# Performance work log

Hardware: AMD Instinct MI355X
Metric: run time of the kernel (lower is better)

Reference implementation:

```python
import jax, jax.numpy as jnp
import numpy as np

H = 128  # hidden_size (hardcoded as hidden_dim=128 in the torch gather)


def _conv1x1(W, b, x):
    # Conv1d kernel_size=1: W [out, in], x [B, in, S] -> [B, out, S]
    return jnp.einsum('oh,bhs->bos', W, x) + b[None, :, None]


def setup_inputs() -> dict:
    key = jax.random.key(0)
    ks = jax.random.split(key, 16)
    B, S = 2048, 128
    sc = 0.05
    inp = {
        'static': jax.random.normal(ks[0], (B, 2, S), jnp.float32),
        'dynamic': jax.random.uniform(ks[1], (B, 2, S), jnp.float32),
        'mark': jnp.zeros((1,), jnp.float32),
        # encoders (Conv1d k=1)
        'W_s': jax.random.normal(ks[2], (H, 2)) * sc, 'b_s': jnp.zeros((H,)),
        'W_ld': jax.random.normal(ks[3], (H, 2)) * sc, 'b_ld': jnp.zeros((H,)),
        'W_d': jax.random.normal(ks[4], (H, 2)) * sc, 'b_d': jnp.zeros((H,)),
        # LSTMCell
        'W_ih': jax.random.normal(ks[5], (4 * H, H)) * sc, 'b_ih': jnp.zeros((4 * H,)),
        'W_hh': jax.random.normal(ks[6], (4 * H, H)) * sc, 'b_hh': jnp.zeros((4 * H,)),
        # pointer projections
        'W_pd': jax.random.normal(ks[7], (H, H)) * sc, 'b_pd': jnp.zeros((H,)),
        'W_pld': jax.random.normal(ks[8], (H, H)) * sc, 'b_pld': jnp.zeros((H,)),
        'W_pq': jax.random.normal(ks[9], (H, H)) * sc, 'b_pq': jnp.zeros((H,)),
        'W_pr': jax.random.normal(ks[10], (H, H)) * sc, 'b_pr': jnp.zeros((H,)),
        # attention vector W (V is unused in the original forward)
        'attn_W': jax.random.normal(ks[11], (1, H)) * sc,
    }
    return inp


def reference(static, dynamic, mark, W_s, b_s, W_ld, b_ld, W_d, b_d,
              W_ih, b_ih, W_hh, b_hh, W_pd, b_pd, W_pld, b_pld,
              W_pq, b_pq, W_pr, b_pr, attn_W):
    B, _, S = static.shape
    static_hidden = _conv1x1(W_s, b_s, static)                 # [B,H,S]
    load, demand = dynamic[:, 0:1, :], dynamic[:, 1:2, :]
    dyn_ld = _conv1x1(W_ld, b_ld, load - demand)               # [B,H,S]
    dyn_d = _conv1x1(W_d, b_d, demand)                         # [B,H,S]
    # loop-invariant projections (recomputed each step in torch; identical math)
    base = (_conv1x1(W_pr, b_pr, static_hidden)
            + _conv1x1(W_pld, b_pld, dyn_ld)
            + _conv1x1(W_pd, b_pd, dyn_d))                     # [B,H,S]

    # mask = [0, 1, 1, ..., 1]; mask_fn is None so it never changes
    mask2 = jnp.concatenate([jnp.zeros((1,), static.dtype),
                             jnp.ones((S - 1,), static.dtype)])

    dec0 = static_hidden[:, :, 0]
    h0 = jnp.zeros((B, H), static.dtype)
    c0 = jnp.zeros((B, H), static.dtype)

    def lstm_cell(x, h, c):
        gates = x @ W_ih.T + b_ih + h @ W_hh.T + b_hh
        i, f, g, o = jnp.split(gates, 4, axis=1)
        c2 = jax.nn.sigmoid(f) * c + jax.nn.sigmoid(i) * jnp.tanh(g)
        h2 = jax.nn.sigmoid(o) * jnp.tanh(c2)
        return h2, c2

    def step(carry, _):
        dec, h, c = carry
        h, c = lstm_cell(dec, h, c)
        q = h @ W_pq.T + b_pq                                  # project_query
        hidden = base + q[:, :, None]                          # [B,H,S]
        attns = jnp.einsum('h,bhs->bs', attn_W[0], jnp.tanh(hidden))
        probs = jax.nn.softmax(attns + 10000.0 * mask2[None, :], axis=1)
        prob = jnp.max(probs, axis=1)                          # greedy (eval path)
        ptr = jnp.argmax(probs, axis=1)
        logp = jnp.log(prob)
        dec2 = jax.lax.stop_gradient(
            jnp.take_along_axis(static_hidden, ptr[:, None, None], axis=2)[:, :, 0])
        return (dec2, h, c), (ptr, logp)

    _, (ptrs, logps) = jax.lax.scan(step, (dec0, h0, c0), None, length=S)
    tour_idx = ptrs.T                                          # [B,S] int
    tour_logp = logps.T                                        # [B,S]
    return tour_idx, tour_logp, mark
```

## Files before the change

kernel.cpp:

```cpp
#include <hip/hip_runtime.h>


#define H 128
#define S 128
#define NBATCH 2048
#define NB 8
#define NT 1024
#define NBLK (NBATCH / NB)
#define BS (NBATCH * S)

#define SHQ 36
#define SHB (4 * SHQ)
#define SHI(bb, h) ((bb) * SHB + (((h) >> 5) * SHQ) + ((h) & 31))
#define QPB 132
#define PADF 12288

typedef float v2f __attribute__((ext_vector_type(2)));
typedef float v4f __attribute__((ext_vector_type(4)));

__device__ __forceinline__ v2f fma2(v2f a, v2f b, v2f c) {
  return __builtin_elementwise_fma(a, b, c);
}
__device__ __forceinline__ v2f splat2(float x) { return (v2f){x, x}; }

__device__ __forceinline__ float dot4f(float4 a, float4 b, float c) {
  return fmaf(a.x, b.x, fmaf(a.y, b.y, fmaf(a.z, b.z, fmaf(a.w, b.w, c))));
}
__device__ __forceinline__ float fast_tanh(float x) {
  float e = __expf(2.f * x);
  float r = __builtin_amdgcn_rcpf(e + 1.f);
  return fmaf(-2.f, r, 1.f);
}
__device__ __forceinline__ float fast_sig(float x) {
  return __builtin_amdgcn_rcpf(1.f + __expf(-x));
}
__device__ __forceinline__ float qsum8(float a) {
  int t;
  t = __builtin_amdgcn_update_dpp(0, __float_as_int(a), 0xB1, 0xF, 0xF, true);
  a += __int_as_float(t);
  t = __builtin_amdgcn_update_dpp(0, __float_as_int(a), 0x4E, 0xF, 0xF, true);
  a += __int_as_float(t);
  a += __shfl_xor(a, 4);
  return a;
}

__global__ __launch_bounds__(NT) __attribute__((amdgpu_waves_per_eu(4, 4)))
void drl4tsp_fused(const float* __restrict__ st, const float* __restrict__ dyn,
                   const float* __restrict__ W_s, const float* __restrict__ b_s,
                   const float* __restrict__ W_ld, const float* __restrict__ b_ld,
                   const float* __restrict__ W_d, const float* __restrict__ b_d,
                   const float* __restrict__ W_ih, const float* __restrict__ b_ih,
                   const float* __restrict__ W_hh, const float* __restrict__ b_hh,
                   const float* __restrict__ W_pd, const float* __restrict__ b_pd,
                   const float* __restrict__ W_pld, const float* __restrict__ b_pld,
                   const float* __restrict__ W_pq, const float* __restrict__ b_pq,
                   const float* __restrict__ W_pr, const float* __restrict__ b_pr,
                   const float* __restrict__ attn_W, const float* __restrict__ mark,
                   float* __restrict__ out)
{
  __shared__ float4 sX[NB][S];
  __shared__ float4 sA[H];
  __shared__ alignas(16) float sAW[H];
  __shared__ float  sQB[H];
  __shared__ float4 sGT4[4][H];
  __shared__ float  sH[NB * SHB];
  __shared__ alignas(16) float sQP[NB * QPB];
  __shared__ float2 sPart[16][64];
  __shared__ float  sOutI[NB][S];
  __shared__ float  sOutL[NB][S];
  __shared__ float  sSelX0[NB];
  __shared__ float  sSelX1[NB];
  __shared__ float  sPad[PADF];

  const int tid = threadIdx.x;
  const int b0  = blockIdx.x * NB;
  const int gg  = tid >> 3, qq = tid & 7;
  const int wv  = tid >> 6, lane = tid & 63;
  const int cb  = wv & 7;
  const int ch  = wv >> 3;

  if (mark[0] > 1e30f) {
    volatile float* vp = sPad;
    vp[tid] = mark[0];
  }

  if (qq == 0) {
    #pragma unroll
    for (int g = 0; g < 4; ++g) {
      const int row = gg + g * H;
      const float* wr = W_ih + row * H;
      float g0 = 0.f, g1 = 0.f, gb = 0.f;
      for (int h = 0; h < H; h += 4) {
        float4 w   = *(const float4*)(wr + h);
        float4 s01 = *(const float4*)(W_s + 2 * h);
        float4 s23 = *(const float4*)(W_s + 2 * h + 4);
        float4 bs  = *(const float4*)(b_s + h);
        g0 = fmaf(w.x, s01.x, fmaf(w.y, s01.z, fmaf(w.z, s23.x, fmaf(w.w, s23.z, g0))));
        g1 = fmaf(w.x, s01.y, fmaf(w.y, s01.w, fmaf(w.z, s23.y, fmaf(w.w, s23.w, g1))));
        gb = fmaf(w.x, bs.x,  fmaf(w.y, bs.y,  fmaf(w.z, bs.z,  fmaf(w.w, bs.w,  gb))));
      }
      sGT4[g][gg] = make_float4(g0, g1, gb + b_ih[row] + b_hh[row], 0.f);
    }
  }
  if (tid < H) {
    const int h = tid;
    float a0 = 0.f, a1 = 0.f, a2 = 0.f, a3 = 0.f, bt = 0.f;
    for (int j = 0; j < H; ++j) {
      float pr  = W_pr[h * H + j];
      float pld = W_pld[h * H + j];
      float pd  = W_pd[h * H + j];
      float2 wsv = *(const float2*)(W_s + 2 * j);
      float2 wld = *(const float2*)(W_ld + 2 * j);
      float2 wd  = *(const float2*)(W_d + 2 * j);
      a0 = fmaf(pr, wsv.x, a0);
      a1 = fmaf(pr, wsv.y, a1);
      a2 = fmaf(pld, wld.x + wld.y, a2);
      a3 = fmaf(pd,  wd.x + wd.y,  a3);
      bt += pr * b_s[j] + pld * b_ld[j] + pd * b_d[j];
    }
    sA[h]  = make_float4(a0, a1, a2, a3);
    sAW[h] = attn_W[h];
    sQB[h] = bt + b_pr[h] + b_pld[h] + b_pd[h] + b_pq[h];
  }
  {
    int i = tid;
    int bb = i >> 7, s = i & (S - 1);
    int go = (b0 + bb) * 2 * S;
    float x0 = st[go + s];
    float x1 = st[go + S + s];
    float ld = dyn[go + s];
    float dm = dyn[go + S + s];
    sX[bb][s] = make_float4(x0, x1, ld - dm, dm);
  }
  for (int i = tid; i < NB * SHB; i += NT) sH[i] = 0.f;
  if (tid < NB) {
    int go = (b0 + tid) * 2 * S;
    sSelX0[tid] = st[go + 0];
    sSelX1[tid] = st[go + S + 0];
  }
  if (blockIdx.x == 0 && tid == 0) out[2 * BS] = mark[0];

  v2f rW01[4][4], rW23[4][4];
  #pragma unroll
  for (int k = 0; k < 4; ++k) {
    const int co = 16 * qq + 4 * k;
    float4 w0 = *(const float4*)(W_hh + (gg        ) * H + co);
    float4 w1 = *(const float4*)(W_hh + (gg +     H) * H + co);
    float4 w2 = *(const float4*)(W_hh + (gg + 2 * H) * H + co);
    float4 w3 = *(const float4*)(W_hh + (gg + 3 * H) * H + co);
    rW01[k][0] = (v2f){w0.x, w1.x}; rW01[k][1] = (v2f){w0.y, w1.y};
    rW01[k][2] = (v2f){w0.z, w1.z}; rW01[k][3] = (v2f){w0.w, w1.w};
    rW23[k][0] = (v2f){w2.x, w3.x}; rW23[k][1] = (v2f){w2.y, w3.y};
    rW23[k][2] = (v2f){w2.z, w3.z}; rW23[k][3] = (v2f){w2.w, w3.w};
  }
  float4 rQ[4];
  {
    const float* wr = W_pq + gg * H + 16 * qq;
    #pragma unroll
    for (int k = 0; k < 4; ++k) rQ[k] = *(const float4*)(wr + 4 * k);
  }
  __syncthreads();

  const int ofsH = ((qq * 16) >> 5) * SHQ + ((qq * 16) & 31);
  const float qb = sQB[gg];
  v2f xx2, xy2, xz2, xw2;
  {
    float4 xA = sX[cb][lane];
    float4 xB = sX[cb][lane + 64];
    xx2 = (v2f){xA.x, xB.x}; xy2 = (v2f){xA.y, xB.y};
    xz2 = (v2f){xA.z, xB.z}; xw2 = (v2f){xA.w, xB.w};
  }
  float cS = 0.f;
  float g4[4] = {0.f, 0.f, 0.f, 0.f};

  #pragma unroll 1
  for (int t = 0; t < S; ++t) {
    {
      const float x0p = sSelX0[qq], x1p = sSelX1[qq];
      float4 t0 = sGT4[0][gg];
      float4 t1 = sGT4[1][gg];
      float4 t2 = sGT4[2][gg];
      float4 t3 = sGT4[3][gg];
      float gi = g4[0] + fmaf(t0.x, x0p, fmaf(t0.y, x1p, t0.z));
      float gf = g4[1] + fmaf(t1.x, x0p, fmaf(t1.y, x1p, t1.z));
      float gc = g4[2] + fmaf(t2.x, x0p, fmaf(t2.y, x1p, t2.z));
      float go = g4[3] + fmaf(t3.x, x0p, fmaf(t3.y, x1p, t3.z));
      cS = fast_sig(gf) * cS + fast_sig(gi) * fast_tanh(gc);
      sH[SHI(qq, gg)] = fast_sig(go) * fast_tanh(cS);
    }
    __syncthreads();

    {
      float qval = 0.f;
      #pragma unroll
      for (int bb = 0; bb < NB; ++bb) {
        float qa = 0.f;
        const float* hp = &sH[bb * SHB + ofsH];
        #pragma unroll
        for (int k = 0; k < 4; ++k)
          qa = dot4f(rQ[k], *(const float4*)(hp + 4 * k), qa);
        qa = qsum8(qa);
        if (qq == bb) qval = qa + qb;
      }
      sQP[qq * QPB + gg] = qval;
    }
    __syncthreads();

    v2f at2 = {0.f, 0.f};
    #pragma unroll 1
    for (int jj = 0; jj < 8; ++jj) {
      v2f a01 = {0.f, 0.f}, a23 = {0.f, 0.f};
      {
        const float* hp = &sH[jj * SHB + ofsH];
        #pragma unroll
        for (int k = 0; k < 4; ++k) {
          v4f hv = *(const v4f*)(hp + 4 * k);
          v2f hx = splat2(hv.x), hy = splat2(hv.y);
          v2f hz = splat2(hv.z), hw = splat2(hv.w);
          a01 = fma2(rW01[k][3], hw, a01);
          a01 = fma2(rW01[k][2], hz, a01);
          a01 = fma2(rW01[k][1], hy, a01);
          a01 = fma2(rW01[k][0], hx, a01);
          a23 = fma2(rW23[k][3], hw, a23);
          a23 = fma2(rW23[k][2], hz, a23);
          a23 = fma2(rW23[k][1], hy, a23);
          a23 = fma2(rW23[k][0], hx, a23);
        }
      }
      {
        const int hbase = 64 * ch + 8 * jj;
        #pragma unroll
        for (int hh = 0; hh < 8; ++hh) {
          const int h = hbase + hh;
          float4 a  = sA[h];
          float  aw = sAW[h];
          float  q  = sQP[cb * QPB + h];
          v2f acc = splat2(q);
          acc = fma2(splat2(a.w), xw2, acc);
          acc = fma2(splat2(a.z), xz2, acc);
          acc = fma2(splat2(a.y), xy2, acc);
          acc = fma2(splat2(a.x), xx2, acc);
          v2f tt = acc + acc;
          v2f e  = (v2f){__expf(tt.x), __expf(tt.y)};
          v2f r  = (v2f){__builtin_amdgcn_rcpf(e.x + 1.f),
                         __builtin_amdgcn_rcpf(e.y + 1.f)};
          v2f th = fma2(splat2(-2.f), r, splat2(1.f));
          at2 = fma2(splat2(aw), th, at2);
        }
      }
      {
        float r0 = qsum8(a01.x);
        float r1 = qsum8(a01.y);
        float r2 = qsum8(a23.x);
        float r3 = qsum8(a23.y);
        if (qq == jj) { g4[0] = r0; g4[1] = r1; g4[2] = r2; g4[3] = r3; }
      }
    }
    sPart[wv][lane] = make_float2(at2.x, at2.y);
    __syncthreads();

    if (wv < 8) {
      float at0 = at2.x, at1 = at2.y;
      float2 o = sPart[wv ^ 8][lane];
      at0 += o.x; at1 += o.y;
      float a0v = at0 + ((lane == 0) ? 0.f : 10000.f);
      float a1v = at1 + 10000.f;
      float v; int idx;
      if (a1v > a0v) { v = a1v; idx = lane + 64; } else { v = a0v; idx = lane; }
      #pragma unroll
      for (int m = 1; m < 64; m <<= 1) {
        float ov = __shfl_xor(v, m);
        int   oi = __shfl_xor(idx, m);
        if (ov > v || (ov == v && oi < idx)) { v = ov; idx = oi; }
      }
      float es = __expf(a0v - v) + __expf(a1v - v);
      #pragma unroll
      for (int m = 1; m < 64; m <<= 1) es += __shfl_xor(es, m);
      if (lane == 0) {
        sOutI[cb][t] = (float)idx;
        sOutL[cb][t] = -__logf(es);
        float4 xv = sX[cb][idx];
        sSelX0[cb] = xv.x;
        sSelX1[cb] = xv.y;
      }
    }
    __syncthreads();
  }

  {
    int bb = tid >> 7, s = tid & (S - 1);
    const int bg = b0 + bb;
    out[bg * S + s]      = sOutI[bb][s];
    out[BS + bg * S + s] = sOutL[bb][s];
  }
}

extern "C" void kernel_launch(void* const* d_in, const int* in_sizes, int n_in,
                              void* d_out, int out_size, void* d_ws, size_t ws_size,
                              hipStream_t stream) {
  const float* st     = (const float*)d_in[0];
  const float* dyn    = (const float*)d_in[1];
  const float* mark   = (const float*)d_in[2];
  const float* W_s    = (const float*)d_in[3];
  const float* b_s    = (const float*)d_in[4];
  const float* W_ld   = (const float*)d_in[5];
  const float* b_ld   = (const float*)d_in[6];
  const float* W_d    = (const float*)d_in[7];
  const float* b_d    = (const float*)d_in[8];
  const float* W_ih   = (const float*)d_in[9];
  const float* b_ih   = (const float*)d_in[10];
  const float* W_hh   = (const float*)d_in[11];
  const float* b_hh   = (const float*)d_in[12];
  const float* W_pd   = (const float*)d_in[13];
  const float* b_pd   = (const float*)d_in[14];
  const float* W_pld  = (const float*)d_in[15];
  const float* b_pld  = (const float*)d_in[16];
  const float* W_pq   = (const float*)d_in[17];
  const float* b_pq   = (const float*)d_in[18];
  const float* W_pr   = (const float*)d_in[19];
  const float* b_pr   = (const float*)d_in[20];
  const float* attn_W = (const float*)d_in[21];
  float* out = (float*)d_out;

  hipLaunchKernelGGL(drl4tsp_fused, dim3(NBLK), dim3(NT), 0, stream,
                     st, dyn, W_s, b_s, W_ld, b_ld, W_d, b_d, W_ih, b_ih,
                     W_hh, b_hh, W_pd, b_pd, W_pld, b_pld, W_pq, b_pq,
                     W_pr, b_pr, attn_W, mark, out);
}
```

Measured before the change: 2.670 ms.

## Move W_hh recurrent matvec after attention, overlapping with argmax reduction phase

The h·W_hh gate matvec is pulled out of the interleaved attention loop and placed after the softmax/argmax section, where it runs in all waves while wave<8 threads finish the reduction. W_hh is now kept as per-gate float4 rows using dot4f instead of packed v2f pairs. The aim is to shorten the attention loop and fill the idle phase before the barrier. In exchange, the attention loop loses the interleaved FMA work that could hide transcendental latency, and register use may change.

```diff
diff --git a/kernel.cpp b/kernel.cpp
--- a/kernel.cpp
+++ b/kernel.cpp
@@ -140,18 +140,12 @@
   }
   if (blockIdx.x == 0 && tid == 0) out[2 * BS] = mark[0];
 
-  v2f rW01[4][4], rW23[4][4];
+  float4 rW[4][4];
   #pragma unroll
-  for (int k = 0; k < 4; ++k) {
-    const int co = 16 * qq + 4 * k;
-    float4 w0 = *(const float4*)(W_hh + (gg        ) * H + co);
-    float4 w1 = *(const float4*)(W_hh + (gg +     H) * H + co);
-    float4 w2 = *(const float4*)(W_hh + (gg + 2 * H) * H + co);
-    float4 w3 = *(const float4*)(W_hh + (gg + 3 * H) * H + co);
-    rW01[k][0] = (v2f){w0.x, w1.x}; rW01[k][1] = (v2f){w0.y, w1.y};
-    rW01[k][2] = (v2f){w0.z, w1.z}; rW01[k][3] = (v2f){w0.w, w1.w};
-    rW23[k][0] = (v2f){w2.x, w3.x}; rW23[k][1] = (v2f){w2.y, w3.y};
-    rW23[k][2] = (v2f){w2.z, w3.z}; rW23[k][3] = (v2f){w2.w, w3.w};
+  for (int g = 0; g < 4; ++g) {
+    const float* wr = W_hh + (gg + g * H) * H + 16 * qq;
+    #pragma unroll
+    for (int k = 0; k < 4; ++k) rW[g][k] = *(const float4*)(wr + 4 * k);
   }
   float4 rQ[4];
   {
@@ -207,53 +201,25 @@
     __syncthreads();
 
     v2f at2 = {0.f, 0.f};
-    #pragma unroll 1
-    for (int jj = 0; jj < 8; ++jj) {
-      v2f a01 = {0.f, 0.f}, a23 = {0.f, 0.f};
-      {
-        const float* hp = &sH[jj * SHB + ofsH];
-        #pragma unroll
-        for (int k = 0; k < 4; ++k) {
-          v4f hv = *(const v4f*)(hp + 4 * k);
-          v2f hx = splat2(hv.x), hy = splat2(hv.y);
-          v2f hz = splat2(hv.z), hw = splat2(hv.w);
-          a01 = fma2(rW01[k][3], hw, a01);
-          a01 = fma2(rW01[k][2], hz, a01);
-          a01 = fma2(rW01[k][1], hy, a01);
-          a01 = fma2(rW01[k][0], hx, a01);
-          a23 = fma2(rW23[k][3], hw, a23);
-          a23 = fma2(rW23[k][2], hz, a23);
-          a23 = fma2(rW23[k][1], hy, a23);
-          a23 = fma2(rW23[k][0], hx, a23);
-        }
-      }
-      {
-        const int hbase = 64 * ch + 8 * jj;
-        #pragma unroll
-        for (int hh = 0; hh < 8; ++hh) {
-          const int h = hbase + hh;
-          float4 a  = sA[h];
-          float  aw = sAW[h];
-          float  q  = sQP[cb * QPB + h];
-          v2f acc = splat2(q);
-          acc = fma2(splat2(a.w), xw2, acc);
-          acc = fma2(splat2(a.z), xz2, acc);
-          acc = fma2(splat2(a.y), xy2, acc);
-          acc = fma2(splat2(a.x), xx2, acc);
-          v2f tt = acc + acc;
-          v2f e  = (v2f){__expf(tt.x), __expf(tt.y)};
-          v2f r  = (v2f){__builtin_amdgcn_rcpf(e.x + 1.f),
-                         __builtin_amdgcn_rcpf(e.y + 1.f)};
-          v2f th = fma2(splat2(-2.f), r, splat2(1.f));
-          at2 = fma2(splat2(aw), th, at2);
-        }
-      }
-      {
-        float r0 = qsum8(a01.x);
-        float r1 = qsum8(a01.y);
-        float r2 = qsum8(a23.x);
-        float r3 = qsum8(a23.y);
-        if (qq == jj) { g4[0] = r0; g4[1] = r1; g4[2] = r2; g4[3] = r3; }
+    {
+      const int hbase = 64 * ch;
+      #pragma unroll 8
+      for (int hh = 0; hh < 64; ++hh) {
+        const int h = hbase + hh;
+        float4 a  = sA[h];
+        float  aw = sAW[h];
+        float  q  = sQP[cb * QPB + h];
+        v2f acc = splat2(q);
+        acc = fma2(splat2(a.w), xw2, acc);
+        acc = fma2(splat2(a.z), xz2, acc);
+        acc = fma2(splat2(a.y), xy2, acc);
+        acc = fma2(splat2(a.x), xx2, acc);
+        v2f tt = acc + acc;
+        v2f e  = (v2f){__expf(tt.x), __expf(tt.y)};
+        v2f r  = (v2f){__builtin_amdgcn_rcpf(e.x + 1.f),
+                       __builtin_amdgcn_rcpf(e.y + 1.f)};
+        v2f th = fma2(splat2(-2.f), r, splat2(1.f));
+        at2 = fma2(splat2(aw), th, at2);
       }
     }
     sPart[wv][lane] = make_float2(at2.x, at2.y);
@@ -282,6 +248,26 @@
         float4 xv = sX[cb][idx];
         sSelX0[cb] = xv.x;
         sSelX1[cb] = xv.y;
+      }
+    }
+    {
+      #pragma unroll
+      for (int bb = 0; bb < NB; ++bb) {
+        float a0 = 0.f, a1 = 0.f, a2 = 0.f, a3 = 0.f;
+        const float* hp = &sH[bb * SHB + ofsH];
+        #pragma unroll
+        for (int k = 0; k < 4; ++k) {
+          float4 hv = *(const float4*)(hp + 4 * k);
+          a0 = dot4f(rW[0][k], hv, a0);
+          a1 = dot4f(rW[1][k], hv, a1);
+          a2 = dot4f(rW[2][k], hv, a2);
+          a3 = dot4f(rW[3][k], hv, a3);
+        }
+        a0 = qsum8(a0);
+        a1 = qsum8(a1);
+        a2 = qsum8(a2);
+        a3 = qsum8(a3);
+        if (qq == bb) { g4[0] = a0; g4[1] = a1; g4[2] = a2; g4[3] = a3; }
       }
     }
     __syncthreads();
```

Measured after the change: 2.313 ms. 1.15x faster.
